# Kernel tuning notes

Hardware: AMD Instinct MI355X
Metric: run time of the kernel (lower is better)

Reference implementation:

```python
import jax, jax.numpy as jnp
import numpy as np

P = 4096      # particles per event
F = 128       # max features per particle (inner ragged axis)
H = 128       # hidden_size


def setup_inputs() -> dict:
    key = jax.random.key(0)
    ks = jax.random.split(key, 12)
    s = 1.0 / np.sqrt(H)  # torch RNN default init scale
    u = lambda k, shp: jax.random.uniform(k, shp, jnp.float32, -s, s)
    event = jax.random.normal(ks[0], (P, F, 1), jnp.float32)
    lengths = jnp.maximum(1, jax.random.randint(ks[1], (P,), 0, F))  # ragged lengths in [1, F)
    return {
        "event": event,
        "lengths": lengths,
        "W_ih1": u(ks[2], (H, 1)), "W_hh1": u(ks[3], (H, H)),
        "b_ih1": u(ks[4], (H,)),   "b_hh1": u(ks[5], (H,)),
        "W_ih2": u(ks[6], (H, H)), "W_hh2": u(ks[7], (H, H)),
        "b_ih2": u(ks[8], (H,)),   "b_hh2": u(ks[9], (H,)),
    }


def reference(event, lengths, W_ih1, W_hh1, b_ih1, b_hh1,
              W_ih2, W_hh2, b_ih2, b_hh2):
    # net1: vanilla tanh RNN over each particle's feature sequence (batched over P).
    # Ragged lengths handled by masking the hidden-state update past each length.
    Pn, Fn, _ = event.shape
    mask = jnp.arange(Fn)[:, None] < lengths[None, :]      # [F, P]
    xs = jnp.transpose(event, (1, 0, 2))                   # [F, P, 1] time-major

    def step1(h, xm):
        x, m = xm                                          # x:[P,1], m:[P]
        h_new = jnp.tanh(x @ W_ih1.T + b_ih1 + h @ W_hh1.T + b_hh1)
        return jnp.where(m[:, None], h_new, h), None

    h0 = jnp.zeros((Pn, H), event.dtype)
    h1, _ = jax.lax.scan(step1, h0, (xs, mask))            # final hidden per particle: [P, H]

    # net2: tanh RNN over the sequence of particle hidden states (unbatched).
    def step2(h, x):
        return jnp.tanh(x @ W_ih2.T + b_ih2 + h @ W_hh2.T + b_hh2), None

    h2, _ = jax.lax.scan(step2, jnp.zeros((H,), event.dtype), h1)
    return h2[None, :]                                     # torch hidden shape (1, H)
```

## Files before the change

kernel.cpp:

```cpp
#include <hip/hip_runtime.h>


constexpr int PN = 4096;
constexpr int FN = 128;
constexpr int HN = 128;
constexpr int CH  = 64;
constexpr int NCH = PN / CH;

__device__ __forceinline__ float fast_tanh(float x) {
    float e = __expf(2.0f * x);
    return 1.0f - 2.0f / (e + 1.0f);
}

__device__ __forceinline__ void lds_barrier() {
    asm volatile("s_waitcnt lgkmcnt(0)\n\ts_barrier" ::: "memory");
}

__device__ __forceinline__ float dpp_xor1(float x) {
    return __int_as_float(__builtin_amdgcn_update_dpp(
        0, __float_as_int(x), 0xB1, 0xF, 0xF, true));
}
__device__ __forceinline__ float dpp_xor2(float x) {
    return __int_as_float(__builtin_amdgcn_update_dpp(
        0, __float_as_int(x), 0x4E, 0xF, 0xF, true));
}
__device__ __forceinline__ float dpp_xor4(float x, bool hi) {
    int a = __builtin_amdgcn_update_dpp(0, __float_as_int(x), 0x104, 0xF, 0xF, true);
    int b = __builtin_amdgcn_update_dpp(0, __float_as_int(x), 0x114, 0xF, 0xF, true);
    return __int_as_float(hi ? b : a);
}
__device__ __forceinline__ float dpp_xor8(float x, bool hi) {
    int a = __builtin_amdgcn_update_dpp(0, __float_as_int(x), 0x108, 0xF, 0xF, true);
    int b = __builtin_amdgcn_update_dpp(0, __float_as_int(x), 0x118, 0xF, 0xF, true);
    return __int_as_float(hi ? b : a);
}

__device__ __forceinline__ float reduce16(const float s[8], int jg) {
    const bool hi8 = (jg & 8) != 0;
    float m0 = hi8 ? s[0] : s[4], k0 = hi8 ? s[4] : s[0];
    float m1 = hi8 ? s[1] : s[5], k1 = hi8 ? s[5] : s[1];
    float m2 = hi8 ? s[2] : s[6], k2 = hi8 ? s[6] : s[2];
    float m3 = hi8 ? s[3] : s[7], k3 = hi8 ? s[7] : s[3];
    float x0 = k0 + dpp_xor8(m0, hi8);
    float x1 = k1 + dpp_xor8(m1, hi8);
    float x2 = k2 + dpp_xor8(m2, hi8);
    float x3 = k3 + dpp_xor8(m3, hi8);
    const bool hi4 = (jg & 4) != 0;
    float y0 = (hi4 ? x2 : x0) + dpp_xor4(hi4 ? x0 : x2, hi4);
    float y1 = (hi4 ? x3 : x1) + dpp_xor4(hi4 ? x1 : x3, hi4);
    const bool hi2 = (jg & 2) != 0;
    float z  = (hi2 ? y1 : y0) + dpp_xor2(hi2 ? y0 : y1);
    z += dpp_xor1(z);
    return z;
}
__device__ __forceinline__ int reduce16_cidx(int jg) {
    return ((jg >> 3) & 1) * 4 + ((jg >> 2) & 1) * 2 + ((jg >> 1) & 1);
}

template <bool SYNC>
__global__ __launch_bounds__(256) void net1_kernel(
    const float* __restrict__ event,
    const int*   __restrict__ lengths,
    const float* __restrict__ W_ih1,
    const float* __restrict__ W_hh1,
    const float* __restrict__ b_ih1,
    const float* __restrict__ b_hh1,
    const float* __restrict__ W_ih2,
    const float* __restrict__ b_ih2,
    const float* __restrict__ b_hh2,
    float* __restrict__ U,
    unsigned*   cnt)
{
    const int p    = blockIdx.x;
    const int tid  = threadIdx.x;
    const int wv   = tid >> 6;
    const int lane = tid & 63;
    const int jg   = lane & 15;
    const int og16 = (wv << 2) + (lane >> 4);
    const int rot  = (jg >> 2) & 1;
    const int oi_w = og16 * 8 + reduce16_cidx(jg);

    __shared__ float h[2][HN];
    __shared__ float ev[FN];

    if (tid < FN) ev[tid]   = event[p * FN + tid];
    if (tid < HN) h[0][tid] = 0.0f;

    float w[8][8];
    #pragma unroll
    for (int c = 0; c < 8; ++c) {
        const float* row = W_hh1 + (og16 * 8 + c) * HN + jg * 8;
        #pragma unroll
        for (int t = 0; t < 2; ++t) {
            const int krot = (t + rot) & 1;
            float4 v = *reinterpret_cast<const float4*>(row + 4 * krot);
            w[c][4*t+0] = v.x; w[c][4*t+1] = v.y;
            w[c][4*t+2] = v.z; w[c][4*t+3] = v.w;
        }
    }
    const float wx_own   = W_ih1[oi_w];
    const float bias_own = b_ih1[oi_w] + b_hh1[oi_w];
    const int   len      = lengths[p];

    __syncthreads();

    for (int t = 0; t < len; ++t) {
        const int cur = t & 1;
        const float x = ev[t];
        const float* base = &h[cur][jg * 8];
        float s[8] = {0,0,0,0,0,0,0,0};
        #pragma unroll
        for (int tt = 0; tt < 2; ++tt) {
            const int krot = (tt + rot) & 1;
            float4 hv = *reinterpret_cast<const float4*>(base + 4 * krot);
            #pragma unroll
            for (int c = 0; c < 8; ++c) {
                s[c] = fmaf(w[c][4*tt+0], hv.x, s[c]);
                s[c] = fmaf(w[c][4*tt+1], hv.y, s[c]);
                s[c] = fmaf(w[c][4*tt+2], hv.z, s[c]);
                s[c] = fmaf(w[c][4*tt+3], hv.w, s[c]);
            }
        }
        const float z  = reduce16(s, jg);
        const float hn = fast_tanh(z + fmaf(wx_own, x, bias_own));
        if ((jg & 1) == 0) h[cur ^ 1][oi_w] = hn;
        lds_barrier();
    }

    if (tid < HN) {
        const float4* h4 = reinterpret_cast<const float4*>(h[len & 1]);
        const float4* w2 = reinterpret_cast<const float4*>(W_ih2 + tid * HN);
        float a0 = b_ih2[tid] + b_hh2[tid], a1 = 0.f, a2 = 0.f, a3 = 0.f;
        #pragma unroll
        for (int k = 0; k < HN / 4; ++k) {
            float4 hv = h4[k];
            float4 wv = w2[k];
            a0 = fmaf(wv.x, hv.x, a0);
            a1 = fmaf(wv.y, hv.y, a1);
            a2 = fmaf(wv.z, hv.z, a2);
            a3 = fmaf(wv.w, hv.w, a3);
        }
        U[p * HN + tid] = (a0 + a1) + (a2 + a3);
    }

    if (SYNC) {
        __syncthreads();
        if (tid == 0) {
            __hip_atomic_fetch_add(&cnt[p >> 6], 1u,
                                   __ATOMIC_RELEASE, __HIP_MEMORY_SCOPE_AGENT);
        }
    }
}

__device__ __forceinline__ void wait_chunk(const unsigned* cnt, int c) {
    while (__hip_atomic_load(&cnt[c], __ATOMIC_ACQUIRE,
                             __HIP_MEMORY_SCOPE_AGENT) < (unsigned)CH) {
        __builtin_amdgcn_s_sleep(8);
    }
}

template <bool SYNC>
__global__ __launch_bounds__(256) void net2_kernel(
    const float* __restrict__ U,
    const float* __restrict__ W_hh2,
    float* __restrict__ out,
    const unsigned* cnt)
{
    const int tid  = threadIdx.x;
    const int wv   = tid >> 6;
    const int lane = tid & 63;
    const int jg   = lane & 7;
    const int ogl  = lane >> 3;
    const int og   = (wv << 3) + ogl;
    const int rot  = jg >> 1;
    const bool hi4 = (jg & 4) != 0;
    const int cidx = ((jg >> 2) & 1) * 2 + ((jg >> 1) & 1);
    const int oi_w = og * 4 + cidx;

    __shared__ float h[2][HN];
    __shared__ float Ulds[2][CH * HN];

    float w[4][16];
    #pragma unroll
    for (int c = 0; c < 4; ++c) {
        const float* row = W_hh2 + (og * 4 + c) * HN + jg * 16;
        #pragma unroll
        for (int t = 0; t < 4; ++t) {
            const int krot = (t + rot) & 3;
            float4 v = *reinterpret_cast<const float4*>(row + 4 * krot);
            w[c][4*t+0] = v.x; w[c][4*t+1] = v.y;
            w[c][4*t+2] = v.z; w[c][4*t+3] = v.w;
        }
    }

    if (SYNC) wait_chunk(cnt, 0);
    {
        const float4* g = reinterpret_cast<const float4*>(U);
        float4*       l = reinterpret_cast<float4*>(&Ulds[0][0]);
        #pragma unroll
        for (int r = 0; r < 8; ++r) l[r * 256 + tid] = g[r * 256 + tid];
    }
    if (tid < HN) h[0][tid] = 0.0f;
    __syncthreads();

    int buf = 0;
    for (int c = 0; c < NCH; ++c) {
        const int nb = buf ^ 1;
        const int cg = (c + 1 < NCH) ? (c + 1) : c;

        if (SYNC) wait_chunk(cnt, cg);

        float4 st[8];
        {
            const float4* gsrc = reinterpret_cast<const float4*>(U + cg * CH * HN);
            #pragma unroll
            for (int r = 0; r < 8; ++r) st[r] = gsrc[r * 256 + tid];
        }

        for (int s2 = 0; s2 < CH; ++s2) {
            const int hc = s2 & 1;
            const float u_cur = Ulds[buf][s2 * HN + oi_w];

            const float* base = &h[hc][jg * 16];
            float s0 = 0.f, s1 = 0.f, s2a = 0.f, s3 = 0.f;
            #pragma unroll
            for (int t = 0; t < 4; ++t) {
                const int krot = (t + rot) & 3;
                float4 hv = *reinterpret_cast<const float4*>(base + 4 * krot);
                s0  = fmaf(w[0][4*t+0], hv.x, s0);  s0  = fmaf(w[0][4*t+1], hv.y, s0);
                s0  = fmaf(w[0][4*t+2], hv.z, s0);  s0  = fmaf(w[0][4*t+3], hv.w, s0);
                s1  = fmaf(w[1][4*t+0], hv.x, s1);  s1  = fmaf(w[1][4*t+1], hv.y, s1);
                s1  = fmaf(w[1][4*t+2], hv.z, s1);  s1  = fmaf(w[1][4*t+3], hv.w, s1);
                s2a = fmaf(w[2][4*t+0], hv.x, s2a); s2a = fmaf(w[2][4*t+1], hv.y, s2a);
                s2a = fmaf(w[2][4*t+2], hv.z, s2a); s2a = fmaf(w[2][4*t+3], hv.w, s2a);
                s3  = fmaf(w[3][4*t+0], hv.x, s3);  s3  = fmaf(w[3][4*t+1], hv.y, s3);
                s3  = fmaf(w[3][4*t+2], hv.z, s3);  s3  = fmaf(w[3][4*t+3], hv.w, s3);
            }

            const bool lo4 = !hi4;
            float t0 = lo4 ? s2a : s0;
            float t1 = lo4 ? s3  : s1;
            float x0 = (lo4 ? s0 : s2a) + dpp_xor4(t0, hi4);
            float x1 = (lo4 ? s1 : s3 ) + dpp_xor4(t1, hi4);
            const bool lo2 = (jg & 2) == 0;
            float t2 = lo2 ? x1 : x0;
            float z  = (lo2 ? x0 : x1) + dpp_xor2(t2);
            z += dpp_xor1(z);

            const float hn = fast_tanh(z + u_cur);
            if ((jg & 1) == 0) h[hc ^ 1][oi_w] = hn;
            lds_barrier();
        }

        {
            float4* ldst = reinterpret_cast<float4*>(&Ulds[nb][0]);
            #pragma unroll
            for (int r = 0; r < 8; ++r) ldst[r * 256 + tid] = st[r];
        }
        __syncthreads();
        buf = nb;
    }

    if (tid < HN) out[tid] = h[0][tid];
}

extern "C" void kernel_launch(void* const* d_in, const int* in_sizes, int n_in,
                              void* d_out, int out_size, void* d_ws, size_t ws_size,
                              hipStream_t stream)
{
    const float* event   = (const float*)d_in[0];
    const int*   lengths = (const int*)  d_in[1];
    const float* W_ih1   = (const float*)d_in[2];
    const float* W_hh1   = (const float*)d_in[3];
    const float* b_ih1   = (const float*)d_in[4];
    const float* b_hh1   = (const float*)d_in[5];
    const float* W_ih2   = (const float*)d_in[6];
    const float* W_hh2   = (const float*)d_in[7];
    const float* b_ih2   = (const float*)d_in[8];
    const float* b_hh2   = (const float*)d_in[9];
    float* out = (float*)d_out;
    float* U   = (float*)d_ws;
    unsigned* cnt = (unsigned*)(U + (size_t)PN * HN);

    const bool sync_ok =
        ws_size >= (size_t)PN * HN * sizeof(float) + NCH * sizeof(unsigned);

    if (sync_ok) {
        hipMemsetAsync(cnt, 0, NCH * sizeof(unsigned), stream);
        net1_kernel<true><<<dim3(PN), dim3(256), 0, stream>>>(
            event, lengths, W_ih1, W_hh1, b_ih1, b_hh1, W_ih2, b_ih2, b_hh2, U, cnt);
        net2_kernel<true><<<dim3(1), dim3(256), 0, stream>>>(U, W_hh2, out, cnt);
    } else {
        net1_kernel<false><<<dim3(PN), dim3(256), 0, stream>>>(
            event, lengths, W_ih1, W_hh1, b_ih1, b_hh1, W_ih2, b_ih2, b_hh2, U, cnt);
        net2_kernel<false><<<dim3(1), dim3(256), 0, stream>>>(U, W_hh2, out, cnt);
    }
}
```

Before: 1.763 ms.

## Fuse net1 and net2 into one kernel so net2 overlaps net1 via counters

Merges the two launches into a single grid where block 0 runs the sequential net2 recurrence and the remaining blocks run net1, synchronised through per-chunk atomic counters. This lets net2 consume chunks of U while net1 is still producing them, instead of waiting for the whole net1 grid. It also single-buffers U in LDS and raises net2's wave priority. The cost is that every block now reserves net2's LDS, which may lower net1 occupancy, and correctness relies on block 0 being resident.

```diff
diff --git a/kernel.cpp b/kernel.cpp
--- a/kernel.cpp
+++ b/kernel.cpp
@@ -57,31 +57,29 @@
     return ((jg >> 3) & 1) * 4 + ((jg >> 2) & 1) * 2 + ((jg >> 1) & 1);
 }
 
+__device__ __forceinline__ void wait_chunk(const unsigned* cnt, int c) {
+    while (__hip_atomic_load(&cnt[c], __ATOMIC_ACQUIRE,
+                             __HIP_MEMORY_SCOPE_AGENT) < (unsigned)CH) {
+        __builtin_amdgcn_s_sleep(8);
+    }
+}
+
 template <bool SYNC>
-__global__ __launch_bounds__(256) void net1_kernel(
-    const float* __restrict__ event,
-    const int*   __restrict__ lengths,
-    const float* __restrict__ W_ih1,
-    const float* __restrict__ W_hh1,
-    const float* __restrict__ b_ih1,
-    const float* __restrict__ b_hh1,
-    const float* __restrict__ W_ih2,
-    const float* __restrict__ b_ih2,
-    const float* __restrict__ b_hh2,
-    float* __restrict__ U,
-    unsigned*   cnt)
-{
-    const int p    = blockIdx.x;
-    const int tid  = threadIdx.x;
+__device__ __forceinline__ void net1_body(
+    int p, int tid,
+    const float* __restrict__ event,  const int* __restrict__ lengths,
+    const float* __restrict__ W_ih1,  const float* __restrict__ W_hh1,
+    const float* __restrict__ b_ih1,  const float* __restrict__ b_hh1,
+    const float* __restrict__ W_ih2,  const float* __restrict__ b_ih2,
+    const float* __restrict__ b_hh2,  float* __restrict__ U,
+    unsigned* cnt, float (*h)[HN], float* ev)
+{
     const int wv   = tid >> 6;
     const int lane = tid & 63;
     const int jg   = lane & 15;
     const int og16 = (wv << 2) + (lane >> 4);
     const int rot  = (jg >> 2) & 1;
     const int oi_w = og16 * 8 + reduce16_cidx(jg);
-
-    __shared__ float h[2][HN];
-    __shared__ float ev[FN];
 
     if (tid < FN) ev[tid]   = event[p * FN + tid];
     if (tid < HN) h[0][tid] = 0.0f;
@@ -152,21 +150,13 @@
     }
 }
 
-__device__ __forceinline__ void wait_chunk(const unsigned* cnt, int c) {
-    while (__hip_atomic_load(&cnt[c], __ATOMIC_ACQUIRE,
-                             __HIP_MEMORY_SCOPE_AGENT) < (unsigned)CH) {
-        __builtin_amdgcn_s_sleep(8);
-    }
-}
-
 template <bool SYNC>
-__global__ __launch_bounds__(256) void net2_kernel(
-    const float* __restrict__ U,
-    const float* __restrict__ W_hh2,
-    float* __restrict__ out,
-    const unsigned* cnt)
-{
-    const int tid  = threadIdx.x;
+__device__ __forceinline__ void net2_body(
+    int tid,
+    const float* __restrict__ U, const float* __restrict__ W_hh2,
+    float* __restrict__ out, const unsigned* cnt,
+    float (*h)[HN], float* Ulds)
+{
     const int wv   = tid >> 6;
     const int lane = tid & 63;
     const int jg   = lane & 7;
@@ -177,8 +167,7 @@
     const int cidx = ((jg >> 2) & 1) * 2 + ((jg >> 1) & 1);
     const int oi_w = og * 4 + cidx;
 
-    __shared__ float h[2][HN];
-    __shared__ float Ulds[2][CH * HN];
+    __builtin_amdgcn_s_setprio(1);
 
     float w[4][16];
     #pragma unroll
@@ -196,30 +185,28 @@
     if (SYNC) wait_chunk(cnt, 0);
     {
         const float4* g = reinterpret_cast<const float4*>(U);
-        float4*       l = reinterpret_cast<float4*>(&Ulds[0][0]);
+        float4*       l = reinterpret_cast<float4*>(Ulds);
         #pragma unroll
         for (int r = 0; r < 8; ++r) l[r * 256 + tid] = g[r * 256 + tid];
     }
     if (tid < HN) h[0][tid] = 0.0f;
     __syncthreads();
 
-    int buf = 0;
     for (int c = 0; c < NCH; ++c) {
-        const int nb = buf ^ 1;
-        const int cg = (c + 1 < NCH) ? (c + 1) : c;
-
-        if (SYNC) wait_chunk(cnt, cg);
+        const bool has_next = (c + 1 < NCH);
+        if (SYNC && has_next) wait_chunk(cnt, c + 1);
 
         float4 st[8];
         {
-            const float4* gsrc = reinterpret_cast<const float4*>(U + cg * CH * HN);
+            const float4* gsrc = reinterpret_cast<const float4*>(
+                U + (has_next ? (c + 1) : c) * CH * HN);
             #pragma unroll
             for (int r = 0; r < 8; ++r) st[r] = gsrc[r * 256 + tid];
         }
 
         for (int s2 = 0; s2 < CH; ++s2) {
             const int hc = s2 & 1;
-            const float u_cur = Ulds[buf][s2 * HN + oi_w];
+            const float u_cur = Ulds[s2 * HN + oi_w];
 
             const float* base = &h[hc][jg * 16];
             float s0 = 0.f, s1 = 0.f, s2a = 0.f, s3 = 0.f;
@@ -251,17 +238,58 @@
             if ((jg & 1) == 0) h[hc ^ 1][oi_w] = hn;
             lds_barrier();
         }
-
-        {
-            float4* ldst = reinterpret_cast<float4*>(&Ulds[nb][0]);
+        if (has_next) {
+            float4* ldst = reinterpret_cast<float4*>(Ulds);
             #pragma unroll
             for (int r = 0; r < 8; ++r) ldst[r * 256 + tid] = st[r];
         }
-        __syncthreads();
-        buf = nb;
+        lds_barrier();
     }
 
     if (tid < HN) out[tid] = h[0][tid];
+}
+
+__global__ __launch_bounds__(256) void fused_kernel(
+    const float* __restrict__ event,  const int* __restrict__ lengths,
+    const float* __restrict__ W_ih1,  const float* __restrict__ W_hh1,
+    const float* __restrict__ b_ih1,  const float* __restrict__ b_hh1,
+    const float* __restrict__ W_ih2,  const float* __restrict__ W_hh2,
+    const float* __restrict__ b_ih2,  const float* __restrict__ b_hh2,
+    float* __restrict__ U, float* __restrict__ out, unsigned* cnt)
+{
+    __shared__ float h[2][HN];
+    __shared__ float ev[FN];
+    __shared__ float Ulds[CH * HN];
+
+    const int tid = threadIdx.x;
+    if (blockIdx.x == 0) {
+        net2_body<true>(tid, U, W_hh2, out, cnt, h, Ulds);
+    } else {
+        net1_body<true>(blockIdx.x - 1, tid, event, lengths, W_ih1, W_hh1,
+                        b_ih1, b_hh1, W_ih2, b_ih2, b_hh2, U, cnt, h, ev);
+    }
+}
+
+__global__ __launch_bounds__(256) void net1_only(
+    const float* __restrict__ event,  const int* __restrict__ lengths,
+    const float* __restrict__ W_ih1,  const float* __restrict__ W_hh1,
+    const float* __restrict__ b_ih1,  const float* __restrict__ b_hh1,
+    const float* __restrict__ W_ih2,  const float* __restrict__ b_ih2,
+    const float* __restrict__ b_hh2,  float* __restrict__ U)
+{
+    __shared__ float h[2][HN];
+    __shared__ float ev[FN];
+    net1_body<false>(blockIdx.x, threadIdx.x, event, lengths, W_ih1, W_hh1,
+                     b_ih1, b_hh1, W_ih2, b_ih2, b_hh2, U, nullptr, h, ev);
+}
+
+__global__ __launch_bounds__(256) void net2_only(
+    const float* __restrict__ U, const float* __restrict__ W_hh2,
+    float* __restrict__ out)
+{
+    __shared__ float h[2][HN];
+    __shared__ float Ulds[CH * HN];
+    net2_body<false>(threadIdx.x, U, W_hh2, out, nullptr, h, Ulds);
 }
 
 extern "C" void kernel_launch(void* const* d_in, const int* in_sizes, int n_in,
@@ -287,12 +315,12 @@
 
     if (sync_ok) {
         hipMemsetAsync(cnt, 0, NCH * sizeof(unsigned), stream);
-        net1_kernel<true><<<dim3(PN), dim3(256), 0, stream>>>(
-            event, lengths, W_ih1, W_hh1, b_ih1, b_hh1, W_ih2, b_ih2, b_hh2, U, cnt);
-        net2_kernel<true><<<dim3(1), dim3(256), 0, stream>>>(U, W_hh2, out, cnt);
+        fused_kernel<<<dim3(PN + 1), dim3(256), 0, stream>>>(
+            event, lengths, W_ih1, W_hh1, b_ih1, b_hh1,
+            W_ih2, W_hh2, b_ih2, b_hh2, U, out, cnt);
     } else {
-        net1_kernel<false><<<dim3(PN), dim3(256), 0, stream>>>(
-            event, lengths, W_ih1, W_hh1, b_ih1, b_hh1, W_ih2, b_ih2, b_hh2, U, cnt);
-        net2_kernel<false><<<dim3(1), dim3(256), 0, stream>>>(U, W_hh2, out, cnt);
-    }
-}
+        net1_only<<<dim3(PN), dim3(256), 0, stream>>>(
+            event, lengths, W_ih1, W_hh1, b_ih1, b_hh1, W_ih2, b_ih2, b_hh2, U);
+        net2_only<<<dim3(1), dim3(256), 0, stream>>>(U, W_hh2, out);
+    }
+}
```

Measured after the change: 1.557 ms. 11.7% less time.
